# Kernel tuning notes

Measured on AMD Instinct MI355X. Metric: run time of the kernel, lower is better.

The kernel has to match this reference:

```python
import jax, jax.numpy as jnp
import numpy as np

N, M, D_IN, D_OUT = 100000, 1024, 64, 64


def setup_inputs() -> dict:
    key = jax.random.key(0)
    ks = jax.random.split(key, 8)
    # kaiming_uniform_ bound for fan_in = D_IN: sqrt(6 / fan_in) with a=sqrt(5) default? torch's
    # kaiming_uniform_ default (a=0) gives bound = sqrt(6/fan_in); exact init is irrelevant for math.
    bound = float(np.sqrt(6.0 / D_IN))
    return {
        "x": jax.random.normal(ks[0], (N, D_IN), dtype=jnp.float32),
        "neighbors": jax.random.normal(ks[1], (M, D_IN), dtype=jnp.float32),
        "Wq": jax.random.uniform(ks[2], (D_OUT, D_IN), jnp.float32, -bound, bound),
        "bq": jnp.zeros((D_OUT,), jnp.float32),
        "Wk": jax.random.uniform(ks[3], (D_OUT, D_IN), jnp.float32, -bound, bound),
        "bk": jnp.zeros((D_OUT,), jnp.float32),
        "Wv": jax.random.uniform(ks[4], (D_OUT, D_IN), jnp.float32, -bound, bound),
        "bv": jnp.zeros((D_OUT,), jnp.float32),
    }


def reference(x, neighbors, Wq, bq, Wk, bk, Wv, bv):
    # q: [N, D_OUT], k: [M, D_OUT]
    q = x @ Wq.T + bq
    k = neighbors @ Wk.T + bk
    # scores: [N, M] -- same math as sum(q[:,None,:] * k[None,:,:], axis=2) but via GEMM
    scores = q @ k.T
    attn = jax.nn.softmax(scores, axis=1)
    # attn @ neighbors: [N, D_IN], then value projection -> [N, D_OUT]
    agg = attn @ neighbors
    return agg @ Wv.T + bv
```

## Files before the change

### kernel.cpp

```cpp
#include <hip/hip_runtime.h>


#define N_ROWS 100000
#define LOG2E 1.44269504088896f
#define GATE_THR 11.5424f

typedef __attribute__((ext_vector_type(8))) _Float16 half8;
typedef __attribute__((ext_vector_type(2))) __fp16   fp16x2;
typedef __attribute__((ext_vector_type(4))) float    f32x4;

#define MFMA16(a,b,c) __builtin_amdgcn_mfma_f32_16x16x32_f16((a),(b),(c),0,0,0)

static __device__ __forceinline__ f32x4 zero4() {
    f32x4 v = {0.f, 0.f, 0.f, 0.f};
    return v;
}

__global__ __launch_bounds__(256)
void prep_kernel(const float* __restrict__ nb, const float* __restrict__ Wq,
                 const float* __restrict__ bq, const float* __restrict__ Wk,
                 unsigned short* __restrict__ GFh, unsigned short* __restrict__ GFl,
                 float* __restrict__ uW, unsigned short* __restrict__ KF,
                 unsigned short* __restrict__ VF)
{
    __shared__ __align__(16) float sm[8192];
    const int tid = threadIdx.x;
    if (blockIdx.x == 0) {
        const float4* wk4 = (const float4*)Wk;
        const float4* wq4 = (const float4*)Wq;
        float4* dk = (float4*)sm;
        float4* dq = (float4*)(sm + 4096);
        #pragma unroll
        for (int u = 0; u < 4; u++) {
            dk[u * 256 + tid] = wk4[u * 256 + tid];
            dq[u * 256 + tid] = wq4[u * 256 + tid];
        }
        __syncthreads();
        const int e2 = tid & 63, e1g = (tid >> 6) * 16;
        float g[16];
        #pragma unroll
        for (int q = 0; q < 16; q++) g[q] = 0.f;
        for (int w = 0; w < 64; w++) {
            float kv = sm[w * 64 + e2];
            const float* wqp = sm + 4096 + w * 64 + e1g;
            #pragma unroll
            for (int q = 0; q < 16; q++) g[q] = fmaf(wqp[q], kv, g[q]);
        }
        union { half8 h; uint4 u; } ph0, pl0, ph1, pl1;
        #pragma unroll
        for (int i = 0; i < 8; i++) {
            _Float16 h0 = (_Float16)g[i];
            ph0.h[i] = h0; pl0.h[i] = (_Float16)(g[i] - (float)h0);
            _Float16 h1 = (_Float16)g[8 + i];
            ph1.h[i] = h1; pl1.h[i] = (_Float16)(g[8 + i] - (float)h1);
        }
        const int mt = e2 >> 4, cc = e2 & 15;
        const int ks = tid >> 7, Q0 = 2 * ((tid >> 6) & 1);
        const int f  = mt * 2 + ks;
        *(uint4*)(GFh + (f * 64 + Q0 * 16 + cc) * 8)       = ph0.u;
        *(uint4*)(GFh + (f * 64 + (Q0 + 1) * 16 + cc) * 8) = ph1.u;
        *(uint4*)(GFl + (f * 64 + Q0 * 16 + cc) * 8)       = pl0.u;
        *(uint4*)(GFl + (f * 64 + (Q0 + 1) * 16 + cc) * 8) = pl1.u;
        if (tid < 64) {
            float uu = 0.f;
            for (int w = 0; w < 64; w++) uu = fmaf(bq[w], sm[w * 64 + tid], uu);
            uW[tid] = uu;
        }
    } else {
        const int T0 = blockIdx.x - 1;
        const int j0 = T0 * 32;
        {
            const int jr = tid >> 3, c0 = (tid & 7) * 8;
            const float* np = nb + (size_t)(j0 + jr) * 64 + c0;
            float4 v0 = *(const float4*)np;
            float4 v1 = *(const float4*)(np + 4);
            sm[jr * 65 + c0 + 0] = v0.x; sm[jr * 65 + c0 + 1] = v0.y;
            sm[jr * 65 + c0 + 2] = v0.z; sm[jr * 65 + c0 + 3] = v0.w;
            sm[jr * 65 + c0 + 4] = v1.x; sm[jr * 65 + c0 + 5] = v1.y;
            sm[jr * 65 + c0 + 6] = v1.z; sm[jr * 65 + c0 + 7] = v1.w;
        }
        {
            const int f = tid >> 6, ln = tid & 63;
            const int t = f >> 1, h = f & 1, Qw = ln >> 4, cw = ln & 15;
            const int key = ((cw >> 3) & 1) * 16 + ((cw >> 2) & 1) * 8 + 4 * t + (cw & 3);
            const float* kp = nb + (size_t)(j0 + key) * 64 + h * 32 + Qw * 8;
            float b[8];
            *(float4*)b       = *(const float4*)kp;
            *(float4*)(b + 4) = *(const float4*)(kp + 4);
            union { half8 hh; uint4 u; } pk;
            #pragma unroll
            for (int i = 0; i < 8; i++) pk.hh[i] = (_Float16)b[i];
            *(uint4*)(KF + (size_t)T0 * 2048 + f * 512 + ln * 8) = pk.u;
        }
        __syncthreads();
        {
            const int dt = tid >> 6, ln = tid & 63;
            const int Qw = ln >> 4, cw = ln & 15;
            union { half8 hh; uint4 u; } pv;
            #pragma unroll
            for (int i = 0; i < 8; i++)
                pv.hh[i] = (_Float16)sm[(Qw * 8 + i) * 65 + dt * 16 + cw];
            *(uint4*)(VF + (size_t)T0 * 2048 + dt * 512 + ln * 8) = pv.u;
        }
    }
}

static __device__ __forceinline__ void flash_step(
    const unsigned short* __restrict__ kfl, const unsigned short* __restrict__ vfl,
    int Tn,
    const half8 (&ck)[4], half8 (&nk)[4], half8 (&vA)[4],
    const half8 (&qh)[2][2], const half8 (&ql)[2][2],
    f32x4 (&acc)[2][4], float (&mrow)[2], float (&lrow)[2])
{
    const unsigned short* kn = kfl + (size_t)Tn * 2048;
    #pragma unroll
    for (int f = 0; f < 4; f++) nk[f] = *(const half8*)(kn + f * 512);

    f32x4 S[2][2];
    __builtin_amdgcn_s_setprio(1);
    #pragma unroll
    for (int t = 0; t < 2; t++)
        #pragma unroll
        for (int qt = 0; qt < 2; qt++) {
            f32x4 s = MFMA16(ck[2 * t],     qh[qt][0], zero4());
            s = MFMA16(ck[2 * t + 1], qh[qt][1], s);
            s = MFMA16(ck[2 * t],     ql[qt][0], s);
            s = MFMA16(ck[2 * t + 1], ql[qt][1], s);
            S[t][qt] = s;
        }
    __builtin_amdgcn_s_setprio(0);

    float pmax[2];
    #pragma unroll
    for (int qt = 0; qt < 2; qt++) {
        pmax[qt] = fmaxf(fmaxf(fmaxf(S[0][qt][0], S[0][qt][1]),
                               fmaxf(S[0][qt][2], S[0][qt][3])),
                         fmaxf(fmaxf(S[1][qt][0], S[1][qt][1]),
                               fmaxf(S[1][qt][2], S[1][qt][3])));
    }
    if (__any((pmax[0] > mrow[0] + GATE_THR) | (pmax[1] > mrow[1] + GATE_THR))) {
        #pragma unroll
        for (int qt = 0; qt < 2; qt++) {
            float cm = pmax[qt];
            cm = fmaxf(cm, __shfl_xor(cm, 16));
            cm = fmaxf(cm, __shfl_xor(cm, 32));
            const float mn = fmaxf(mrow[qt], cm);
            const float sc = __builtin_amdgcn_exp2f(mrow[qt] - mn);
            mrow[qt] = mn;
            lrow[qt] *= sc;
            #pragma unroll
            for (int dt = 0; dt < 4; dt++)
                #pragma unroll
                for (int r = 0; r < 4; r++) acc[qt][dt][r] *= sc;
        }
    }
    union { half8 v; fp16x2 h2[4]; } pk[2];
    #pragma unroll
    for (int qt = 0; qt < 2; qt++) {
        const float mref = mrow[qt];
        float p[8];
        #pragma unroll
        for (int r = 0; r < 4; r++) {
            p[r]     = __builtin_amdgcn_exp2f(S[0][qt][r] - mref);
            p[4 + r] = __builtin_amdgcn_exp2f(S[1][qt][r] - mref);
        }
        lrow[qt] += ((p[0] + p[1]) + (p[2] + p[3])) + ((p[4] + p[5]) + (p[6] + p[7]));
        #pragma unroll
        for (int j = 0; j < 4; j++)
            pk[qt].h2[j] = __builtin_amdgcn_cvt_pkrtz(p[2 * j], p[2 * j + 1]);
    }
    __builtin_amdgcn_s_setprio(1);
    #pragma unroll
    for (int dt = 0; dt < 4; dt++) {
        acc[0][dt] = MFMA16(vA[dt], pk[0].v, acc[0][dt]);
        acc[1][dt] = MFMA16(vA[dt], pk[1].v, acc[1][dt]);
    }
    __builtin_amdgcn_s_setprio(0);
    const unsigned short* vn = vfl + (size_t)Tn * 2048;
    #pragma unroll
    for (int d = 0; d < 4; d++) vA[d] = *(const half8*)(vn + d * 512);
}

__global__ __launch_bounds__(64, 3)
void attn_kernel(const float* __restrict__ x,
                 const unsigned short* __restrict__ GFh,
                 const unsigned short* __restrict__ GFl,
                 const float* __restrict__ uW,
                 const unsigned short* __restrict__ KF,
                 const unsigned short* __restrict__ VF,
                 const float* __restrict__ Wv,
                 const float* __restrict__ bv,
                 float* __restrict__ out)
{
    __shared__ __align__(16) float slice[1088];
    const int lane = threadIdx.x & 63;
    const int Q    = lane >> 4;
    const int c    = lane & 15;
    const int rbase = blockIdx.x * 32;

    half8 qh[2][2], ql[2][2];
    #pragma unroll
    for (int rt = 0; rt < 2; rt++) {
        const int row = rbase + rt * 16 + c;
        half8 xh[2], xl[2];
        #pragma unroll
        for (int ks = 0; ks < 2; ks++) {
            const float* xp = x + (size_t)row * 64 + ks * 32 + Q * 8;
            float a[8];
            *(float4*)a       = *(const float4*)xp;
            *(float4*)(a + 4) = *(const float4*)(xp + 4);
            #pragma unroll
            for (int i = 0; i < 8; i++) {
                _Float16 h = (_Float16)a[i];
                xh[ks][i] = h;
                xl[ks][i] = (_Float16)(a[i] - (float)h);
            }
        }
        #pragma unroll
        for (int mt = 0; mt < 4; mt++) {
            f32x4 Cm = zero4();
            #pragma unroll
            for (int ks = 0; ks < 2; ks++) {
                half8 gh = *(const half8*)(GFh + ((mt * 2 + ks) * 64 + lane) * 8);
                half8 gl = *(const half8*)(GFl + ((mt * 2 + ks) * 64 + lane) * 8);
                Cm = MFMA16(gh, xh[ks], Cm);
                Cm = MFMA16(gh, xl[ks], Cm);
                Cm = MFMA16(gl, xh[ks], Cm);
            }
            *(f32x4*)(slice + c * 68 + mt * 16 + 4 * Q) = Cm;
        }
        __builtin_amdgcn_s_waitcnt(0);
        #pragma unroll
        for (int ks = 0; ks < 2; ks++) {
            const float* qp = slice + c * 68 + ks * 32 + Q * 8;
            const float* up = uW + ks * 32 + Q * 8;
            #pragma unroll
            for (int i = 0; i < 8; i++) {
                float val = (qp[i] + up[i]) * LOG2E;
                _Float16 h = (_Float16)val;
                qh[rt][ks][i] = h;
                ql[rt][ks][i] = (_Float16)(val - (float)h);
            }
        }
        __builtin_amdgcn_s_waitcnt(0);
    }

    f32x4 acc[2][4];
    #pragma unroll
    for (int qt = 0; qt < 2; qt++)
        #pragma unroll
        for (int dt = 0; dt < 4; dt++) acc[qt][dt] = zero4();
    float mrow[2] = { -3.0e38f, -3.0e38f };
    float lrow[2] = { 0.f, 0.f };

    const unsigned short* kfl = KF + lane * 8;
    const unsigned short* vfl = VF + lane * 8;
    half8 kA[4], kB[4], vA[4];
    #pragma unroll
    for (int f = 0; f < 4; f++) kA[f] = *(const half8*)(kfl + f * 512);
    #pragma unroll
    for (int d = 0; d < 4; d++) vA[d] = *(const half8*)(vfl + d * 512);

    #pragma unroll 1
    for (int TT = 0; TT < 16; TT++) {
        flash_step(kfl, vfl, 2 * TT + 1, kA, kB, vA, qh, ql, acc, mrow, lrow);
        const int Tn = (2 * TT + 2 < 32) ? 2 * TT + 2 : 31;
        flash_step(kfl, vfl, Tn,         kB, kA, vA, qh, ql, acc, mrow, lrow);
    }

    #pragma unroll
    for (int qt = 0; qt < 2; qt++) {
        float l = lrow[qt];
        l += __shfl_xor(l, 16);
        l += __shfl_xor(l, 32);
        const float rl = 1.f / l;
        #pragma unroll
        for (int dt = 0; dt < 4; dt++)
            #pragma unroll
            for (int r = 0; r < 4; r++) acc[qt][dt][r] *= rl;
    }
    half8 wf[4][2];
    #pragma unroll
    for (int mt = 0; mt < 4; mt++)
        #pragma unroll
        for (int ks = 0; ks < 2; ks++) {
            const float* wp = Wv + (size_t)(mt * 16 + c) * 64 + ks * 32 + Q * 8;
            #pragma unroll
            for (int i = 0; i < 8; i++) wf[mt][ks][i] = (_Float16)wp[i];
        }
    const int srcA = 32 * (Q & 1) + c;
    const int srcB = srcA + 16;
    const bool hi = (Q >> 1) & 1;
    f32x4 o[2][4];
    #pragma unroll
    for (int qt = 0; qt < 2; qt++) {
        half8 pe[2];
        #pragma unroll
        for (int ks = 0; ks < 2; ks++) {
            #pragma unroll
            for (int r = 0; r < 4; r++) {
                float a0 = __shfl(acc[qt][2 * ks + 0][r], srcA);
                float a1 = __shfl(acc[qt][2 * ks + 1][r], srcA);
                float b0 = __shfl(acc[qt][2 * ks + 0][r], srcB);
                float b1 = __shfl(acc[qt][2 * ks + 1][r], srcB);
                pe[ks][r]     = (_Float16)(hi ? a1 : a0);
                pe[ks][4 + r] = (_Float16)(hi ? b1 : b0);
            }
        }
        #pragma unroll
        for (int mt = 0; mt < 4; mt++) {
            f32x4 t = MFMA16(wf[mt][0], pe[0], zero4());
            o[qt][mt] = MFMA16(wf[mt][1], pe[1], t);
        }
    }
    #pragma unroll
    for (int qt = 0; qt < 2; qt++) {
        const int row = rbase + qt * 16 + c;
        #pragma unroll
        for (int mt = 0; mt < 4; mt++) {
            const float4 bf = *(const float4*)(bv + mt * 16 + 4 * Q);
            float4 vv = make_float4(o[qt][mt][0] + bf.x, o[qt][mt][1] + bf.y,
                                    o[qt][mt][2] + bf.z, o[qt][mt][3] + bf.w);
            *(float4*)(out + (size_t)row * 64 + mt * 16 + 4 * Q) = vv;
        }
    }
}

extern "C" void kernel_launch(void* const* d_in, const int* in_sizes, int n_in,
                              void* d_out, int out_size, void* d_ws, size_t ws_size,
                              hipStream_t stream)
{
    const float* x  = (const float*)d_in[0];
    const float* nb = (const float*)d_in[1];
    const float* Wq = (const float*)d_in[2];
    const float* bq = (const float*)d_in[3];
    const float* Wk = (const float*)d_in[4];
    const float* Wv = (const float*)d_in[6];
    const float* bv = (const float*)d_in[7];
    float* out = (float*)d_out;

    char* ws = (char*)d_ws;
    unsigned short* GFh = (unsigned short*)(ws);
    unsigned short* GFl = (unsigned short*)(ws + 8192);
    float*          uW  = (float*)(ws + 16384);
    unsigned short* KF  = (unsigned short*)(ws + 16640);
    unsigned short* VF  = (unsigned short*)(ws + 147712);

    prep_kernel<<<33, 256, 0, stream>>>(nb, Wq, bq, Wk, GFh, GFl, uW, KF, VF);
    const int grid = N_ROWS / 32;
    attn_kernel<<<grid, 64, 0, stream>>>(x, GFh, GFl, uW, KF, VF, Wv, bv, out);
}
```

Before: 149.2 us.

## Split key loop across two waves per block and merge softmax partials

Each block now runs two waves on the same 32 query rows, and each wave processes half of the key/value tiles. The partial accumulators, maxima and sums from the second wave are passed through shared memory and merged by the first wave with an online-softmax rescale before the value projection. This shortens each wave's serial loop and raises the number of waves, with the aim of better latency hiding. In exchange, each wave repeats the query projection, and the merge adds block synchronisation and shared-memory traffic.

```diff
diff --git a/kernel.cpp b/kernel.cpp
--- a/kernel.cpp
+++ b/kernel.cpp
@@ -181,7 +181,7 @@
     for (int d = 0; d < 4; d++) vA[d] = *(const half8*)(vn + d * 512);
 }
 
-__global__ __launch_bounds__(64, 3)
+__global__ __launch_bounds__(128, 3)
 void attn_kernel(const float* __restrict__ x,
                  const unsigned short* __restrict__ GFh,
                  const unsigned short* __restrict__ GFl,
@@ -192,11 +192,14 @@
                  const float* __restrict__ bv,
                  float* __restrict__ out)
 {
-    __shared__ __align__(16) float slice[1088];
-    const int lane = threadIdx.x & 63;
+    __shared__ __align__(16) float smf[2304];
+    const int tid  = threadIdx.x;
+    const int lane = tid & 63;
+    const int wv   = tid >> 6;
     const int Q    = lane >> 4;
     const int c    = lane & 15;
     const int rbase = blockIdx.x * 32;
+    float* slice = smf + wv * 1088;
 
     half8 qh[2][2], ql[2][2];
     #pragma unroll
@@ -255,73 +258,97 @@
 
     const unsigned short* kfl = KF + lane * 8;
     const unsigned short* vfl = VF + lane * 8;
+    const int TB = wv * 16;
     half8 kA[4], kB[4], vA[4];
     #pragma unroll
-    for (int f = 0; f < 4; f++) kA[f] = *(const half8*)(kfl + f * 512);
-    #pragma unroll
-    for (int d = 0; d < 4; d++) vA[d] = *(const half8*)(vfl + d * 512);
+    for (int f = 0; f < 4; f++) kA[f] = *(const half8*)(kfl + (size_t)TB * 2048 + f * 512);
+    #pragma unroll
+    for (int d = 0; d < 4; d++) vA[d] = *(const half8*)(vfl + (size_t)TB * 2048 + d * 512);
 
     #pragma unroll 1
-    for (int TT = 0; TT < 16; TT++) {
-        flash_step(kfl, vfl, 2 * TT + 1, kA, kB, vA, qh, ql, acc, mrow, lrow);
-        const int Tn = (2 * TT + 2 < 32) ? 2 * TT + 2 : 31;
-        flash_step(kfl, vfl, Tn,         kB, kA, vA, qh, ql, acc, mrow, lrow);
-    }
-
+    for (int i = 0; i < 8; i++) {
+        flash_step(kfl, vfl, TB + 2 * i + 1, kA, kB, vA, qh, ql, acc, mrow, lrow);
+        const int Tn = (2 * i + 2 < 16) ? TB + 2 * i + 2 : TB + 15;
+        flash_step(kfl, vfl, Tn,             kB, kA, vA, qh, ql, acc, mrow, lrow);
+    }
+
+    float mfull[2], lfull[2];
     #pragma unroll
     for (int qt = 0; qt < 2; qt++) {
         float l = lrow[qt];
         l += __shfl_xor(l, 16);
         l += __shfl_xor(l, 32);
-        const float rl = 1.f / l;
-        #pragma unroll
-        for (int dt = 0; dt < 4; dt++)
-            #pragma unroll
-            for (int r = 0; r < 4; r++) acc[qt][dt][r] *= rl;
-    }
-    half8 wf[4][2];
-    #pragma unroll
-    for (int mt = 0; mt < 4; mt++)
-        #pragma unroll
-        for (int ks = 0; ks < 2; ks++) {
-            const float* wp = Wv + (size_t)(mt * 16 + c) * 64 + ks * 32 + Q * 8;
-            #pragma unroll
-            for (int i = 0; i < 8; i++) wf[mt][ks][i] = (_Float16)wp[i];
-        }
-    const int srcA = 32 * (Q & 1) + c;
-    const int srcB = srcA + 16;
-    const bool hi = (Q >> 1) & 1;
-    f32x4 o[2][4];
-    #pragma unroll
-    for (int qt = 0; qt < 2; qt++) {
-        half8 pe[2];
-        #pragma unroll
-        for (int ks = 0; ks < 2; ks++) {
-            #pragma unroll
-            for (int r = 0; r < 4; r++) {
-                float a0 = __shfl(acc[qt][2 * ks + 0][r], srcA);
-                float a1 = __shfl(acc[qt][2 * ks + 1][r], srcA);
-                float b0 = __shfl(acc[qt][2 * ks + 0][r], srcB);
-                float b1 = __shfl(acc[qt][2 * ks + 1][r], srcB);
-                pe[ks][r]     = (_Float16)(hi ? a1 : a0);
-                pe[ks][4 + r] = (_Float16)(hi ? b1 : b0);
-            }
-        }
-        #pragma unroll
-        for (int mt = 0; mt < 4; mt++) {
-            f32x4 t = MFMA16(wf[mt][0], pe[0], zero4());
-            o[qt][mt] = MFMA16(wf[mt][1], pe[1], t);
-        }
-    }
-    #pragma unroll
-    for (int qt = 0; qt < 2; qt++) {
-        const int row = rbase + qt * 16 + c;
-        #pragma unroll
-        for (int mt = 0; mt < 4; mt++) {
-            const float4 bf = *(const float4*)(bv + mt * 16 + 4 * Q);
-            float4 vv = make_float4(o[qt][mt][0] + bf.x, o[qt][mt][1] + bf.y,
-                                    o[qt][mt][2] + bf.z, o[qt][mt][3] + bf.w);
-            *(float4*)(out + (size_t)row * 64 + mt * 16 + 4 * Q) = vv;
+        lfull[qt] = l;
+        mfull[qt] = mrow[qt];
+    }
+
+    __syncthreads();
+    if (wv == 1) {
+        #pragma unroll
+        for (int qt = 0; qt < 2; qt++) {
+            #pragma unroll
+            for (int dt = 0; dt < 4; dt++)
+                *(f32x4*)(smf + (qt * 4 + dt) * 256 + lane * 4) = acc[qt][dt];
+            smf[2048 + qt * 64 + lane]       = mfull[qt];
+            smf[2048 + 128 + qt * 64 + lane] = lfull[qt];
+        }
+    }
+    __syncthreads();
+    if (wv == 0) {
+        #pragma unroll
+        for (int qt = 0; qt < 2; qt++) {
+            const float m1 = smf[2048 + qt * 64 + lane];
+            const float l1 = smf[2048 + 128 + qt * 64 + lane];
+            const float mn = fmaxf(mfull[qt], m1);
+            const float f0 = __builtin_amdgcn_exp2f(mfull[qt] - mn);
+            const float f1 = __builtin_amdgcn_exp2f(m1 - mn);
+            const float rl = 1.f / (lfull[qt] * f0 + l1 * f1);
+            const float g0 = f0 * rl, g1 = f1 * rl;
+            #pragma unroll
+            for (int dt = 0; dt < 4; dt++) {
+                const f32x4 a1 = *(const f32x4*)(smf + (qt * 4 + dt) * 256 + lane * 4);
+                #pragma unroll
+                for (int r = 0; r < 4; r++)
+                    acc[qt][dt][r] = acc[qt][dt][r] * g0 + a1[r] * g1;
+            }
+        }
+        half8 wf[4][2];
+        #pragma unroll
+        for (int mt = 0; mt < 4; mt++)
+            #pragma unroll
+            for (int ks = 0; ks < 2; ks++) {
+                const float* wp = Wv + (size_t)(mt * 16 + c) * 64 + ks * 32 + Q * 8;
+                #pragma unroll
+                for (int i = 0; i < 8; i++) wf[mt][ks][i] = (_Float16)wp[i];
+            }
+        const int srcA = 32 * (Q & 1) + c;
+        const int srcB = srcA + 16;
+        const bool hi = (Q >> 1) & 1;
+        #pragma unroll
+        for (int qt = 0; qt < 2; qt++) {
+            half8 pe[2];
+            #pragma unroll
+            for (int ks = 0; ks < 2; ks++) {
+                #pragma unroll
+                for (int r = 0; r < 4; r++) {
+                    float a0 = __shfl(acc[qt][2 * ks + 0][r], srcA);
+                    float a1 = __shfl(acc[qt][2 * ks + 1][r], srcA);
+                    float b0 = __shfl(acc[qt][2 * ks + 0][r], srcB);
+                    float b1 = __shfl(acc[qt][2 * ks + 1][r], srcB);
+                    pe[ks][r]     = (_Float16)(hi ? a1 : a0);
+                    pe[ks][4 + r] = (_Float16)(hi ? b1 : b0);
+                }
+            }
+            const int row = rbase + qt * 16 + c;
+            #pragma unroll
+            for (int mt = 0; mt < 4; mt++) {
+                f32x4 t = MFMA16(wf[mt][0], pe[0], zero4());
+                f32x4 o = MFMA16(wf[mt][1], pe[1], t);
+                const float4 bf = *(const float4*)(bv + mt * 16 + 4 * Q);
+                float4 vv = make_float4(o[0] + bf.x, o[1] + bf.y,
+                                        o[2] + bf.z, o[3] + bf.w);
+                *(float4*)(out + (size_t)row * 64 + mt * 16 + 4 * Q) = vv;
+            }
         }
     }
 }
@@ -348,5 +375,5 @@
 
     prep_kernel<<<33, 256, 0, stream>>>(nb, Wq, bq, Wk, GFh, GFl, uW, KF, VF);
     const int grid = N_ROWS / 32;
-    attn_kernel<<<grid, 64, 0, stream>>>(x, GFh, GFl, uW, KF, VF, Wv, bv, out);
-}
+    attn_kernel<<<grid, 128, 0, stream>>>(x, GFh, GFl, uW, KF, VF, Wv, bv, out);
+}
```

Measured after the change: 154.3 us. 3.4% more time.
